# Kernel tuning notes

Measured on AMD Instinct MI355X. Metric: run time of the kernel, lower is better.

The kernel has to match this reference:

```python
import jax, jax.numpy as jnp
import numpy as np

B, N, C, H, W = 32, 32, 3, 32, 32
HID, OUT = 256, 128


def _conv(x, w, b):
    y = jax.lax.conv_general_dilated(
        x, w, window_strides=(1, 1), padding="SAME",
        dimension_numbers=("NCHW", "OIHW", "NCHW"))
    return y + b[None, :, None, None]


def _sage(h, lw, lb, rw):
    # PyG SAGEConv with mean aggregation on a fully-connected graph (no self-loops):
    # agg_i = (sum_j h_j - h_i) / (N-1); out = agg @ lw.T + lb + h @ rw.T
    n = h.shape[1]
    agg = (jnp.sum(h, axis=1, keepdims=True) - h) / (n - 1)
    return jnp.einsum('bnd,od->bno', agg, lw) + lb + jnp.einsum('bnd,od->bno', h, rw)


def setup_inputs() -> dict:
    key = jax.random.key(0)
    ks = jax.random.split(key, 16)
    def g(k, shape, scale):
        return jax.random.normal(k, shape, dtype=jnp.float32) * scale
    return {
        "x": jax.random.normal(ks[0], (B, N, C, H, W), dtype=jnp.float32),
        "mask": jnp.ones((B, N), dtype=jnp.float32),
        "conv1_w": g(ks[1], (64, C, 3, 3), 0.1),
        "conv1_b": jnp.zeros((64,), jnp.float32),
        "conv2_w": g(ks[2], (128, 64, 3, 3), 0.05),
        "conv2_b": jnp.zeros((128,), jnp.float32),
        "fc_w": g(ks[3], (HID, 128), 0.08),
        "fc_b": jnp.zeros((HID,), jnp.float32),
        "s1_lw": g(ks[4], (HID, HID), 0.06),
        "s1_lb": jnp.zeros((HID,), jnp.float32),
        "s1_rw": g(ks[5], (HID, HID), 0.06),
        "s2_lw": g(ks[6], (OUT, HID), 0.06),
        "s2_lb": jnp.zeros((OUT,), jnp.float32),
        "s2_rw": g(ks[7], (OUT, HID), 0.06),
    }


def reference(x, mask, conv1_w, conv1_b, conv2_w, conv2_b, fc_w, fc_b,
              s1_lw, s1_lb, s1_rw, s2_lw, s2_lb, s2_rw):
    b, n, c, h, w = x.shape
    z = x.reshape(b * n, c, h, w)
    z = jax.nn.relu(_conv(z, conv1_w, conv1_b))
    z = jax.nn.relu(_conv(z, conv2_w, conv2_b))
    z = jnp.mean(z, axis=(2, 3))                      # AdaptiveAvgPool2d((1,1)) + flatten
    z = z @ fc_w.T + fc_b                             # [B*N, HID]
    z = z.reshape(b, n, -1) * mask[:, :, None]
    z = jax.nn.relu(_sage(z, s1_lw, s1_lb, s1_rw))
    z = _sage(z, s2_lw, s2_lb, s2_rw)                 # [B, N, OUT]
    return z
```

## Files before the change

### kernel.cpp

```cpp
#include <hip/hip_runtime.h>
#include <hip/hip_bf16.h>


typedef __attribute__((ext_vector_type(8))) short bfrag;
typedef __attribute__((ext_vector_type(4))) float f32x4;
typedef __attribute__((ext_vector_type(16))) float f32x16;

static __device__ __forceinline__ unsigned short f2bf(float f) {
    union { float f; unsigned u; } v; v.f = f;
    unsigned r = v.u + 0x7fff + ((v.u >> 16) & 1);
    return (unsigned short)(r >> 16);
}

__global__ __launch_bounds__(256) void prep_kernel(
    const float* __restrict__ s1lw, const float* __restrict__ s1rw,
    const float* __restrict__ s2lw, const float* __restrict__ s2rw,
    const float* __restrict__ c2w, const float* __restrict__ c1w,
    const float* __restrict__ c1b, const float* __restrict__ fcw,
    float* __restrict__ l1T, float* __restrict__ w1pT,
    float* __restrict__ l2T, float* __restrict__ w2pT,
    float* __restrict__ fwT,
    short* __restrict__ w2c, short* __restrict__ w1b) {
    int i = blockIdx.x * 256 + threadIdx.x;
    const float inv31 = 1.f / 31.f;
    if (i < 65536) {
        int d = i >> 8, o = i & 255;
        float lw = s1lw[o * 256 + d];
        l1T[i]  = lw;
        w1pT[i] = s1rw[o * 256 + d] - lw * inv31;
    }
    if (i < 32768) {
        int d = i >> 7, o = i & 127;
        float lw = s2lw[o * 256 + d];
        l2T[i]  = lw;
        w2pT[i] = s2rw[o * 256 + d] - lw * inv31;
        int c = i >> 8, o2 = i & 255;
        fwT[i] = fcw[o2 * 128 + c];
    }
    if (i < 73728) {
        int tap = i >> 13, r = i & 8191;
        int ks = r >> 11, hi = (r >> 10) & 1, oc = (r >> 3) & 127, j = i & 7;
        int ic = ks * 16 + hi * 8 + j;
        w2c[i] = (short)f2bf(c2w[(oc * 64 + ic) * 9 + tap]);
    }
    if (i < 2048) {
        int oc = i >> 5, k = i & 31;
        float v = (k < 27) ? c1w[oc * 27 + k] : (k == 27 ? c1b[oc] : 0.f);
        w1b[i] = (short)f2bf(v);
    }
}

__global__ __launch_bounds__(256, 2) void fused_conv_kernel(
    const float* __restrict__ x, const short* __restrict__ w1b,
    const short* __restrict__ w2c, const float* __restrict__ b2,
    float* __restrict__ pooled4) {
    const int band = blockIdx.x, img = blockIdx.y;
    __shared__ short xt[3 * 12 * 34];
    __shared__ short c1t[10 * 34 * 72];
    __shared__ float wsum[4][128];
    const int t = threadIdx.x;
    const int w = t >> 6, lane = t & 63;
    const int ln15 = lane & 15, q8 = (lane >> 4) * 8;
    const int ln31 = lane & 31, hi = lane >> 5;

    const float* xi = x + img * 3072;
    for (int idx = t; idx < 1224; idx += 256) {
        int c = idx / 408, rem = idx % 408, r = rem / 34, col = rem % 34;
        int y = band * 8 - 2 + r, xx = col - 1;
        float v = 0.f;
        if ((unsigned)y < 32u && (unsigned)xx < 32u) v = xi[c * 1024 + y * 32 + xx];
        xt[idx] = (short)f2bf(v);
    }
    {
        f32x4 z = {0.f, 0.f, 0.f, 0.f};
        for (int i = t; i < 180; i += 256) {
            int r = i / 18, rem = i % 18, side = rem / 9, q = rem % 9;
            *(f32x4*)(c1t + (r * 34 + side * 33) * 72 + q * 8) = z;
        }
    }
    bfrag b1f[4];
#pragma unroll
    for (int ot = 0; ot < 4; ++ot)
        b1f[ot] = *(const bfrag*)(w1b + (ot * 16 + ln15) * 32 + q8);

    int xOff[8]; int kMask[8]; int kOvr[8];
#pragma unroll
    for (int j = 0; j < 8; ++j) {
        int k = q8 + j;
        int c = (k * 57) >> 9;
        int rem = k - 9 * c;
        int dy = (rem * 11) >> 5;
        int dx = rem - 3 * dy;
        int cc = c < 3 ? c : 2;
        xOff[j] = cc * 408 + dy * 34 + dx;
        kMask[j] = (c < 3) ? 0xFFFF : 0;
        kOvr[j]  = (c < 3) ? 0 : (k == 27 ? 0x3F80 : 0);
    }
    __syncthreads();

#pragma unroll 1
    for (int pt = 0; pt < 5; ++pt) {
        const int tile = w * 5 + pt;
        const int posA = tile * 16 + ln15;
        const int baseA = (posA >> 5) * 34 + (posA & 31);
        bfrag a1f;
#pragma unroll
        for (int j = 0; j < 8; ++j)
            a1f[j] = (short)((xt[xOff[j] + baseA] & kMask[j]) | kOvr[j]);
        f32x4 acc1[4];
#pragma unroll
        for (int ot = 0; ot < 4; ++ot) {
#pragma unroll
            for (int rg = 0; rg < 4; ++rg) acc1[ot][rg] = 0.f;
            acc1[ot] = __builtin_amdgcn_mfma_f32_16x16x32_bf16(
                a1f, b1f[ot], acc1[ot], 0, 0, 0);
        }
#pragma unroll
        for (int rg = 0; rg < 4; ++rg) {
            int pos = tile * 16 + (lane >> 4) * 4 + rg;
            int r = pos >> 5, xc = pos & 31;
            int y = band * 8 - 1 + r;
            bool valid = (unsigned)y < 32u;
#pragma unroll
            for (int ot = 0; ot < 4; ++ot) {
                float v = fmaxf(acc1[ot][rg], 0.f);
                c1t[(r * 34 + xc + 1) * 72 + ot * 16 + ln15] =
                    valid ? (short)f2bf(v) : (short)0;
            }
        }
    }
    __syncthreads();

    float b2v[4];
#pragma unroll
    for (int ot = 0; ot < 4; ++ot) b2v[ot] = b2[ot * 32 + ln31];

    f32x16 acc[2][4];
#pragma unroll
    for (int pt = 0; pt < 2; ++pt)
#pragma unroll
        for (int ot = 0; ot < 4; ++ot)
#pragma unroll
            for (int rg = 0; rg < 16; ++rg) acc[pt][ot][rg] = 0.f;

    const int aB0 = (w * 2 * 34 + ln31) * 72 + hi * 8;
    const int aB1 = aB0 + 34 * 72;
    const short* bPtr = w2c + hi * 1024 + ln31 * 8;

    bfrag aX[4], bX[8], aY[4], bY[8];
    auto loadS = [&](bfrag* af, bfrag* bf, int st) {
        const int tap = st >> 1, kh = st & 1;
        const int dy = (tap * 11) >> 5, dx = tap - 3 * dy;
        const int dOff = (dy * 34 + dx) * 72 + kh * 32;
        af[0] = *(const bfrag*)&c1t[aB0 + dOff];
        af[1] = *(const bfrag*)&c1t[aB0 + dOff + 16];
        af[2] = *(const bfrag*)&c1t[aB1 + dOff];
        af[3] = *(const bfrag*)&c1t[aB1 + dOff + 16];
        const short* p = bPtr + st * 4096;
#pragma unroll
        for (int kk = 0; kk < 2; ++kk)
#pragma unroll
            for (int ot = 0; ot < 4; ++ot)
                bf[kk * 4 + ot] = *(const bfrag*)(p + kk * 2048 + ot * 256);
    };
    auto computeS = [&](const bfrag* af, const bfrag* bf) {
#pragma unroll
        for (int kk = 0; kk < 2; ++kk)
#pragma unroll
            for (int pt = 0; pt < 2; ++pt)
#pragma unroll
                for (int ot = 0; ot < 4; ++ot)
                    acc[pt][ot] = __builtin_amdgcn_mfma_f32_32x32x16_bf16(
                        af[pt * 2 + kk], bf[kk * 4 + ot], acc[pt][ot], 0, 0, 0);
    };

    loadS(aX, bX, 0);
#pragma unroll 1
    for (int st = 0; st < 18; st += 2) {
        loadS(aY, bY, st + 1);
        computeS(aX, bX);
        if (st + 2 < 18) loadS(aX, bX, st + 2);
        computeS(aY, bY);
    }

#pragma unroll
    for (int ot = 0; ot < 4; ++ot) {
        float s = 0.f;
#pragma unroll
        for (int pt = 0; pt < 2; ++pt)
#pragma unroll
            for (int rg = 0; rg < 16; ++rg)
                s += fmaxf(acc[pt][ot][rg] + b2v[ot], 0.f);
        s += __shfl_xor(s, 32, 64);
        if (lane < 32) wsum[w][ot * 32 + ln31] = s;
    }
    __syncthreads();
    if (t < 128) {
        pooled4[((size_t)img * 4 + band) * 128 + t] =
            wsum[0][t] + wsum[1][t] + wsum[2][t] + wsum[3][t];
    }
}

__global__ __launch_bounds__(256) void fc_kernel(
    const float* __restrict__ pooled4, const float* __restrict__ fwT,
    const float* __restrict__ fb, const float* __restrict__ mask,
    float* __restrict__ z1) {
    const int img = blockIdx.x;
    __shared__ float m[128];
    const int t = threadIdx.x;
    if (t < 128) {
        const float* p = pooled4 + (size_t)img * 4 * 128 + t;
        m[t] = (p[0] + p[128] + p[256] + p[384]) * (1.f / 1024.f);
    }
    __syncthreads();
    float acc = fb[t];
#pragma unroll 4
    for (int c = 0; c < 128; ++c) acc = fmaf(m[c], fwT[c * 256 + t], acc);
    z1[img * 256 + t] = acc * mask[img];
}

__global__ __launch_bounds__(256) void sage1_kernel(
    const float* __restrict__ z1, const float* __restrict__ l1T,
    const float* __restrict__ lb, const float* __restrict__ w1pT,
    float* __restrict__ z2) {
    const int bb = blockIdx.x >> 3, chunk = blockIdx.x & 7;
    __shared__ float h[32 * 256];
    __shared__ float sl[256];
    const int t = threadIdx.x;
    const float* zb = z1 + bb * 8192;
    for (int idx = t; idx < 8192; idx += 256) h[idx] = zb[idx];
    __syncthreads();
    float s = 0.f;
#pragma unroll
    for (int n = 0; n < 32; ++n) s += h[n * 256 + t];
    sl[t] = s * (1.f / 31.f);
    __syncthreads();
    float c = lb[t];
#pragma unroll 4
    for (int d = 0; d < 256; ++d) c = fmaf(sl[d], l1T[d * 256 + t], c);
    float acc[4];
#pragma unroll
    for (int i = 0; i < 4; ++i) acc[i] = c;
    for (int d0 = 0; d0 < 256; d0 += 4) {
        float wv0 = w1pT[(d0 + 0) * 256 + t];
        float wv1 = w1pT[(d0 + 1) * 256 + t];
        float wv2 = w1pT[(d0 + 2) * 256 + t];
        float wv3 = w1pT[(d0 + 3) * 256 + t];
#pragma unroll
        for (int i = 0; i < 4; ++i) {
            f32x4 hv = *(const f32x4*)&h[(chunk * 4 + i) * 256 + d0];
            acc[i] = fmaf(hv[0], wv0, acc[i]);
            acc[i] = fmaf(hv[1], wv1, acc[i]);
            acc[i] = fmaf(hv[2], wv2, acc[i]);
            acc[i] = fmaf(hv[3], wv3, acc[i]);
        }
    }
    for (int i = 0; i < 4; ++i)
        z2[(bb * 32 + chunk * 4 + i) * 256 + t] = fmaxf(acc[i], 0.f);
}

__global__ __launch_bounds__(256) void sage2_kernel(
    const float* __restrict__ z2, const float* __restrict__ l2T,
    const float* __restrict__ lb, const float* __restrict__ w2pT,
    float* __restrict__ out) {
    const int bb = blockIdx.x >> 3, chunk = blockIdx.x & 7;
    __shared__ float h[32 * 256];
    __shared__ float sl[256];
    const int t = threadIdx.x;
    const float* zb = z2 + bb * 8192;
    for (int idx = t; idx < 8192; idx += 256) h[idx] = zb[idx];
    __syncthreads();
    float s = 0.f;
#pragma unroll
    for (int n = 0; n < 32; ++n) s += h[n * 256 + t];
    sl[t] = s * (1.f / 31.f);
    __syncthreads();
    const int o = t & 127, half = t >> 7;
    float c = lb[o];
#pragma unroll 4
    for (int d = 0; d < 256; ++d) c = fmaf(sl[d], l2T[d * 128 + o], c);
    float acc[2];
    acc[0] = c; acc[1] = c;
    const int n0 = chunk * 4 + half * 2;
    for (int d0 = 0; d0 < 256; d0 += 4) {
        float wv0 = w2pT[(d0 + 0) * 128 + o];
        float wv1 = w2pT[(d0 + 1) * 128 + o];
        float wv2 = w2pT[(d0 + 2) * 128 + o];
        float wv3 = w2pT[(d0 + 3) * 128 + o];
#pragma unroll
        for (int ii = 0; ii < 2; ++ii) {
            f32x4 hv = *(const f32x4*)&h[(n0 + ii) * 256 + d0];
            acc[ii] = fmaf(hv[0], wv0, acc[ii]);
            acc[ii] = fmaf(hv[1], wv1, acc[ii]);
            acc[ii] = fmaf(hv[2], wv2, acc[ii]);
            acc[ii] = fmaf(hv[3], wv3, acc[ii]);
        }
    }
    for (int ii = 0; ii < 2; ++ii)
        out[(size_t)(bb * 32 + n0 + ii) * 128 + o] = acc[ii];
}

extern "C" void kernel_launch(void* const* d_in, const int* in_sizes, int n_in,
                              void* d_out, int out_size, void* d_ws, size_t ws_size,
                              hipStream_t stream) {
    const float* x    = (const float*)d_in[0];
    const float* mask = (const float*)d_in[1];
    const float* c1w  = (const float*)d_in[2];
    const float* c1b  = (const float*)d_in[3];
    const float* c2w  = (const float*)d_in[4];
    const float* c2b  = (const float*)d_in[5];
    const float* fcw  = (const float*)d_in[6];
    const float* fcb  = (const float*)d_in[7];
    const float* s1lw = (const float*)d_in[8];
    const float* s1lb = (const float*)d_in[9];
    const float* s1rw = (const float*)d_in[10];
    const float* s2lw = (const float*)d_in[11];
    const float* s2lb = (const float*)d_in[12];
    const float* s2rw = (const float*)d_in[13];
    float* out = (float*)d_out;

    char* ws = (char*)d_ws;
    float* pooled4 = (float*)(ws);
    float* z1      = (float*)(ws + 2048u * 1024);
    float* z2      = (float*)(ws + 3072u * 1024);
    float* l1T     = (float*)(ws + 4096u * 1024);
    float* w1pT    = (float*)(ws + 4352u * 1024);
    float* l2T     = (float*)(ws + 4608u * 1024);
    float* w2pT    = (float*)(ws + 4736u * 1024);
    float* fwT     = (float*)(ws + 4864u * 1024);
    short* w2c     = (short*)(ws + 4992u * 1024);
    short* w1b     = (short*)(ws + 5136u * 1024);

    prep_kernel<<<dim3(288), 256, 0, stream>>>(s1lw, s1rw, s2lw, s2rw, c2w, c1w, c1b,
                                               fcw, l1T, w1pT, l2T, w2pT, fwT, w2c, w1b);
    fused_conv_kernel<<<dim3(4, 1024), 256, 0, stream>>>(x, w1b, w2c, c2b, pooled4);
    fc_kernel<<<dim3(1024), 256, 0, stream>>>(pooled4, fwT, fcb, mask, z1);
    sage1_kernel<<<dim3(256), 256, 0, stream>>>(z1, l1T, s1lb, w1pT, z2);
    sage2_kernel<<<dim3(256), 256, 0, stream>>>(z2, l2T, s2lb, w2pT, out);
}
```

Before: 288.3 us.

## Halve conv band height, accumulate pooled sums atomically, batch fc over images

```diff
diff --git a/kernel.cpp b/kernel.cpp
--- a/kernel.cpp
+++ b/kernel.cpp
@@ -20,7 +20,8 @@
     float* __restrict__ l1T, float* __restrict__ w1pT,
     float* __restrict__ l2T, float* __restrict__ w2pT,
     float* __restrict__ fwT,
-    short* __restrict__ w2c, short* __restrict__ w1b) {
+    short* __restrict__ w2c, short* __restrict__ w1b,
+    float* __restrict__ pooled) {
     int i = blockIdx.x * 256 + threadIdx.x;
     const float inv31 = 1.f / 31.f;
     if (i < 65536) {
@@ -28,6 +29,8 @@
         float lw = s1lw[o * 256 + d];
         l1T[i]  = lw;
         w1pT[i] = s1rw[o * 256 + d] - lw * inv31;
+        pooled[i] = 0.f;
+        pooled[i + 65536] = 0.f;
     }
     if (i < 32768) {
         int d = i >> 7, o = i & 127;
@@ -50,13 +53,13 @@
     }
 }
 
-__global__ __launch_bounds__(256, 2) void fused_conv_kernel(
+__global__ __launch_bounds__(256, 3) void fused_conv_kernel(
     const float* __restrict__ x, const short* __restrict__ w1b,
     const short* __restrict__ w2c, const float* __restrict__ b2,
-    float* __restrict__ pooled4) {
+    float* __restrict__ pooled) {
     const int band = blockIdx.x, img = blockIdx.y;
-    __shared__ short xt[3 * 12 * 34];
-    __shared__ short c1t[10 * 34 * 72];
+    __shared__ short xt[3 * 8 * 34];
+    __shared__ short c1t[6 * 34 * 72];
     __shared__ float wsum[4][128];
     const int t = threadIdx.x;
     const int w = t >> 6, lane = t & 63;
@@ -64,16 +67,16 @@
     const int ln31 = lane & 31, hi = lane >> 5;
 
     const float* xi = x + img * 3072;
-    for (int idx = t; idx < 1224; idx += 256) {
-        int c = idx / 408, rem = idx % 408, r = rem / 34, col = rem % 34;
-        int y = band * 8 - 2 + r, xx = col - 1;
+    for (int idx = t; idx < 816; idx += 256) {
+        int c = idx / 272, rem = idx % 272, r = rem / 34, col = rem % 34;
+        int y = band * 4 - 2 + r, xx = col - 1;
         float v = 0.f;
         if ((unsigned)y < 32u && (unsigned)xx < 32u) v = xi[c * 1024 + y * 32 + xx];
         xt[idx] = (short)f2bf(v);
     }
     {
         f32x4 z = {0.f, 0.f, 0.f, 0.f};
-        for (int i = t; i < 180; i += 256) {
+        for (int i = t; i < 108; i += 256) {
             int r = i / 18, rem = i % 18, side = rem / 9, q = rem % 9;
             *(f32x4*)(c1t + (r * 34 + side * 33) * 72 + q * 8) = z;
         }
@@ -92,15 +95,15 @@
         int dy = (rem * 11) >> 5;
         int dx = rem - 3 * dy;
         int cc = c < 3 ? c : 2;
-        xOff[j] = cc * 408 + dy * 34 + dx;
+        xOff[j] = cc * 272 + dy * 34 + dx;
         kMask[j] = (c < 3) ? 0xFFFF : 0;
         kOvr[j]  = (c < 3) ? 0 : (k == 27 ? 0x3F80 : 0);
     }
     __syncthreads();
 
 #pragma unroll 1
-    for (int pt = 0; pt < 5; ++pt) {
-        const int tile = w * 5 + pt;
+    for (int pt = 0; pt < 3; ++pt) {
+        const int tile = w * 3 + pt;
         const int posA = tile * 16 + ln15;
         const int baseA = (posA >> 5) * 34 + (posA & 31);
         bfrag a1f;
@@ -119,7 +122,7 @@
         for (int rg = 0; rg < 4; ++rg) {
             int pos = tile * 16 + (lane >> 4) * 4 + rg;
             int r = pos >> 5, xc = pos & 31;
-            int y = band * 8 - 1 + r;
+            int y = band * 4 - 1 + r;
             bool valid = (unsigned)y < 32u;
 #pragma unroll
             for (int ot = 0; ot < 4; ++ot) {
@@ -135,27 +138,17 @@
 #pragma unroll
     for (int ot = 0; ot < 4; ++ot) b2v[ot] = b2[ot * 32 + ln31];
 
-    f32x16 acc[2][4];
-#pragma unroll
-    for (int pt = 0; pt < 2; ++pt)
-#pragma unroll
-        for (int ot = 0; ot < 4; ++ot)
-#pragma unroll
-            for (int rg = 0; rg < 16; ++rg) acc[pt][ot][rg] = 0.f;
-
-    const int aB0 = (w * 2 * 34 + ln31) * 72 + hi * 8;
-    const int aB1 = aB0 + 34 * 72;
+    f32x16 acc[4];
+#pragma unroll
+    for (int ot = 0; ot < 4; ++ot)
+#pragma unroll
+        for (int rg = 0; rg < 16; ++rg) acc[ot][rg] = 0.f;
+
+    const int aB0 = (w * 34 + ln31) * 72 + hi * 8;
     const short* bPtr = w2c + hi * 1024 + ln31 * 8;
 
-    bfrag aX[4], bX[8], aY[4], bY[8];
-    auto loadS = [&](bfrag* af, bfrag* bf, int st) {
-        const int tap = st >> 1, kh = st & 1;
-        const int dy = (tap * 11) >> 5, dx = tap - 3 * dy;
-        const int dOff = (dy * 34 + dx) * 72 + kh * 32;
-        af[0] = *(const bfrag*)&c1t[aB0 + dOff];
-        af[1] = *(const bfrag*)&c1t[aB0 + dOff + 16];
-        af[2] = *(const bfrag*)&c1t[aB1 + dOff];
-        af[3] = *(const bfrag*)&c1t[aB1 + dOff + 16];
+    bfrag bX[8], bY[8];
+    auto loadB = [&](bfrag* bf, int st) {
         const short* p = bPtr + st * 4096;
 #pragma unroll
         for (int kk = 0; kk < 2; ++kk)
@@ -163,60 +156,73 @@
             for (int ot = 0; ot < 4; ++ot)
                 bf[kk * 4 + ot] = *(const bfrag*)(p + kk * 2048 + ot * 256);
     };
-    auto computeS = [&](const bfrag* af, const bfrag* bf) {
-#pragma unroll
-        for (int kk = 0; kk < 2; ++kk)
-#pragma unroll
-            for (int pt = 0; pt < 2; ++pt)
-#pragma unroll
-                for (int ot = 0; ot < 4; ++ot)
-                    acc[pt][ot] = __builtin_amdgcn_mfma_f32_32x32x16_bf16(
-                        af[pt * 2 + kk], bf[kk * 4 + ot], acc[pt][ot], 0, 0, 0);
+    auto computeS = [&](int st, const bfrag* bf) {
+        const int tap = st >> 1, kh = st & 1;
+        const int dy = (tap * 11) >> 5, dx = tap - 3 * dy;
+        const int a0 = aB0 + (dy * 34 + dx) * 72 + kh * 32;
+        bfrag af0 = *(const bfrag*)&c1t[a0];
+        bfrag af1 = *(const bfrag*)&c1t[a0 + 16];
+#pragma unroll
+        for (int ot = 0; ot < 4; ++ot)
+            acc[ot] = __builtin_amdgcn_mfma_f32_32x32x16_bf16(
+                af0, bf[ot], acc[ot], 0, 0, 0);
+#pragma unroll
+        for (int ot = 0; ot < 4; ++ot)
+            acc[ot] = __builtin_amdgcn_mfma_f32_32x32x16_bf16(
+                af1, bf[4 + ot], acc[ot], 0, 0, 0);
     };
 
-    loadS(aX, bX, 0);
+    loadB(bX, 0);
 #pragma unroll 1
     for (int st = 0; st < 18; st += 2) {
-        loadS(aY, bY, st + 1);
-        computeS(aX, bX);
-        if (st + 2 < 18) loadS(aX, bX, st + 2);
-        computeS(aY, bY);
+        loadB(bY, st + 1);
+        computeS(st, bX);
+        if (st + 2 < 18) loadB(bX, st + 2);
+        computeS(st + 1, bY);
     }
 
 #pragma unroll
     for (int ot = 0; ot < 4; ++ot) {
         float s = 0.f;
 #pragma unroll
-        for (int pt = 0; pt < 2; ++pt)
-#pragma unroll
-            for (int rg = 0; rg < 16; ++rg)
-                s += fmaxf(acc[pt][ot][rg] + b2v[ot], 0.f);
+        for (int rg = 0; rg < 16; ++rg)
+            s += fmaxf(acc[ot][rg] + b2v[ot], 0.f);
         s += __shfl_xor(s, 32, 64);
         if (lane < 32) wsum[w][ot * 32 + ln31] = s;
     }
     __syncthreads();
     if (t < 128) {
-        pooled4[((size_t)img * 4 + band) * 128 + t] =
-            wsum[0][t] + wsum[1][t] + wsum[2][t] + wsum[3][t];
+        atomicAdd(&pooled[(size_t)img * 128 + t],
+                  wsum[0][t] + wsum[1][t] + wsum[2][t] + wsum[3][t]);
     }
 }
 
 __global__ __launch_bounds__(256) void fc_kernel(
-    const float* __restrict__ pooled4, const float* __restrict__ fwT,
+    const float* __restrict__ pooled, const float* __restrict__ fwT,
     const float* __restrict__ fb, const float* __restrict__ mask,
     float* __restrict__ z1) {
-    const int img = blockIdx.x;
-    __shared__ float m[128];
+    const int g = blockIdx.x;
+    __shared__ float m[4][128];
     const int t = threadIdx.x;
     if (t < 128) {
-        const float* p = pooled4 + (size_t)img * 4 * 128 + t;
-        m[t] = (p[0] + p[128] + p[256] + p[384]) * (1.f / 1024.f);
-    }
-    __syncthreads();
-    float acc = fb[t];
+#pragma unroll
+        for (int i = 0; i < 4; ++i)
+            m[i][t] = pooled[(size_t)(g * 4 + i) * 128 + t] * (1.f / 1024.f);
+    }
+    __syncthreads();
+    float a0 = fb[t], a1 = a0, a2 = a0, a3 = a0;
 #pragma unroll 4
-    for (int c = 0; c < 128; ++c) acc = fmaf(m[c], fwT[c * 256 + t], acc);
-    z1[img * 256 + t] = acc * mask[img];
+    for (int c = 0; c < 128; ++c) {
+        float wv = fwT[c * 256 + t];
+        a0 = fmaf(m[0][c], wv, a0);
+        a1 = fmaf(m[1][c], wv, a1);
+        a2 = fmaf(m[2][c], wv, a2);
+        a3 = fmaf(m[3][c], wv, a3);
+    }
+    z1[(g * 4 + 0) * 256 + t] = a0 * mask[g * 4 + 0];
+    z1[(g * 4 + 1) * 256 + t] = a1 * mask[g * 4 + 1];
+    z1[(g * 4 + 2) * 256 + t] = a2 * mask[g * 4 + 2];
+    z1[(g * 4 + 3) * 256 + t] = a3 * mask[g * 4 + 3];
 }
 
 __global__ __launch_bounds__(256) void sage1_kernel(
@@ -320,7 +326,7 @@
     float* out = (float*)d_out;
 
     char* ws = (char*)d_ws;
-    float* pooled4 = (float*)(ws);
+    float* pooled  = (float*)(ws);
     float* z1      = (float*)(ws + 2048u * 1024);
     float* z2      = (float*)(ws + 3072u * 1024);
     float* l1T     = (float*)(ws + 4096u * 1024);
@@ -332,9 +338,10 @@
     short* w1b     = (short*)(ws + 5136u * 1024);
 
     prep_kernel<<<dim3(288), 256, 0, stream>>>(s1lw, s1rw, s2lw, s2rw, c2w, c1w, c1b,
-                                               fcw, l1T, w1pT, l2T, w2pT, fwT, w2c, w1b);
-    fused_conv_kernel<<<dim3(4, 1024), 256, 0, stream>>>(x, w1b, w2c, c2b, pooled4);
-    fc_kernel<<<dim3(1024), 256, 0, stream>>>(pooled4, fwT, fcb, mask, z1);
+                                               fcw, l1T, w1pT, l2T, w2pT, fwT, w2c, w1b,
+                                               pooled);
+    fused_conv_kernel<<<dim3(8, 1024), 256, 0, stream>>>(x, w1b, w2c, c2b, pooled);
+    fc_kernel<<<dim3(256), 256, 0, stream>>>(pooled, fwT, fcb, mask, z1);
     sage1_kernel<<<dim3(256), 256, 0, stream>>>(z1, l1T, s1lb, w1pT, z2);
     sage2_kernel<<<dim3(256), 256, 0, stream>>>(z2, l2T, s2lb, w2pT, out);
 }
```

New measurement: 313.1 us. +8.6%, slower.

## Stage conv2 weights through triple-buffered LDS and pack conv1 bf16 stores

Applied to the files above, without the earlier changes.

```diff
diff --git a/kernel.cpp b/kernel.cpp
--- a/kernel.cpp
+++ b/kernel.cpp
@@ -10,6 +10,18 @@
     union { float f; unsigned u; } v; v.f = f;
     unsigned r = v.u + 0x7fff + ((v.u >> 16) & 1);
     return (unsigned short)(r >> 16);
+}
+
+static __device__ __forceinline__ unsigned cvtpk(float lo, float hi) {
+    unsigned r;
+    asm("v_cvt_pk_bf16_f32 %0, %1, %2" : "=v"(r) : "v"(lo), "v"(hi));
+    return r;
+}
+
+static __device__ __forceinline__ void gl_lds16(const short* g, short* l) {
+    __builtin_amdgcn_global_load_lds(
+        (const __attribute__((address_space(1))) unsigned int*)g,
+        (__attribute__((address_space(3))) unsigned int*)l, 16, 0, 0);
 }
 
 __global__ __launch_bounds__(256) void prep_kernel(
@@ -57,6 +69,7 @@
     const int band = blockIdx.x, img = blockIdx.y;
     __shared__ short xt[3 * 12 * 34];
     __shared__ short c1t[10 * 34 * 72];
+    __shared__ short bufB[3][4096];
     __shared__ float wsum[4][128];
     const int t = threadIdx.x;
     const int w = t >> 6, lane = t & 63;
@@ -98,11 +111,20 @@
     }
     __syncthreads();
 
+    {
+        const short* src = w2c + t * 8;
+        short* dst = (short*)bufB + t * 8;
+        gl_lds16(src, dst);
+        gl_lds16(src + 2048, dst + 2048);
+        gl_lds16(src + 4096, dst + 4096);
+        gl_lds16(src + 6144, dst + 6144);
+    }
+
 #pragma unroll 1
     for (int pt = 0; pt < 5; ++pt) {
         const int tile = w * 5 + pt;
-        const int posA = tile * 16 + ln15;
-        const int baseA = (posA >> 5) * 34 + (posA & 31);
+        const int r = tile >> 1, xcb = (tile & 1) << 4;
+        const int baseA = r * 34 + xcb + ln15;
         bfrag a1f;
 #pragma unroll
         for (int j = 0; j < 8; ++j)
@@ -113,20 +135,19 @@
 #pragma unroll
             for (int rg = 0; rg < 4; ++rg) acc1[ot][rg] = 0.f;
             acc1[ot] = __builtin_amdgcn_mfma_f32_16x16x32_bf16(
-                a1f, b1f[ot], acc1[ot], 0, 0, 0);
-        }
-#pragma unroll
-        for (int rg = 0; rg < 4; ++rg) {
-            int pos = tile * 16 + (lane >> 4) * 4 + rg;
-            int r = pos >> 5, xc = pos & 31;
-            int y = band * 8 - 1 + r;
-            bool valid = (unsigned)y < 32u;
-#pragma unroll
-            for (int ot = 0; ot < 4; ++ot) {
-                float v = fmaxf(acc1[ot][rg], 0.f);
-                c1t[(r * 34 + xc + 1) * 72 + ot * 16 + ln15] =
-                    valid ? (short)f2bf(v) : (short)0;
+                b1f[ot], a1f, acc1[ot], 0, 0, 0);
+        }
+        const int y = band * 8 - 1 + r;
+        const bool valid = (unsigned)y < 32u;
+        const int waddr = (r * 34 + xcb + ln15 + 1) * 72 + (lane >> 4) * 4;
+#pragma unroll
+        for (int ot = 0; ot < 4; ++ot) {
+            uint2 pk = {0u, 0u};
+            if (valid) {
+                pk.x = cvtpk(fmaxf(acc1[ot][0], 0.f), fmaxf(acc1[ot][1], 0.f));
+                pk.y = cvtpk(fmaxf(acc1[ot][2], 0.f), fmaxf(acc1[ot][3], 0.f));
             }
+            *(uint2*)&c1t[waddr + ot * 16] = pk;
         }
     }
     __syncthreads();
@@ -145,42 +166,54 @@
 
     const int aB0 = (w * 2 * 34 + ln31) * 72 + hi * 8;
     const int aB1 = aB0 + 34 * 72;
-    const short* bPtr = w2c + hi * 1024 + ln31 * 8;
-
-    bfrag aX[4], bX[8], aY[4], bY[8];
-    auto loadS = [&](bfrag* af, bfrag* bf, int st) {
+    const int bOff = hi * 1024 + ln31 * 8;
+    const short* stSrc = w2c + t * 8;
+    short* stDst = (short*)bufB + t * 8;
+
+    int rb = 0;
+#pragma unroll 1
+    for (int st = 0; st < 18; ++st) {
+        if (st + 2 < 18) {
+            const int sb = (rb >= 1) ? rb - 1 : 2;
+            const short* src = stSrc + (st + 2) * 4096;
+            short* dst = stDst + sb * 4096;
+            gl_lds16(src, dst);
+            gl_lds16(src + 2048, dst + 2048);
+        }
         const int tap = st >> 1, kh = st & 1;
         const int dy = (tap * 11) >> 5, dx = tap - 3 * dy;
-        const int dOff = (dy * 34 + dx) * 72 + kh * 32;
-        af[0] = *(const bfrag*)&c1t[aB0 + dOff];
-        af[1] = *(const bfrag*)&c1t[aB0 + dOff + 16];
-        af[2] = *(const bfrag*)&c1t[aB1 + dOff];
-        af[3] = *(const bfrag*)&c1t[aB1 + dOff + 16];
-        const short* p = bPtr + st * 4096;
+        const int aOff = (dy * 34 + dx) * 72 + kh * 32;
+        const short* bc = (const short*)bufB + rb * 4096 + bOff;
+        bfrag af0 = *(const bfrag*)&c1t[aB0 + aOff];
+        bfrag af1 = *(const bfrag*)&c1t[aB0 + aOff + 16];
+        bfrag af2 = *(const bfrag*)&c1t[aB1 + aOff];
+        bfrag af3 = *(const bfrag*)&c1t[aB1 + aOff + 16];
+        bfrag bf[8];
 #pragma unroll
         for (int kk = 0; kk < 2; ++kk)
 #pragma unroll
             for (int ot = 0; ot < 4; ++ot)
-                bf[kk * 4 + ot] = *(const bfrag*)(p + kk * 2048 + ot * 256);
-    };
-    auto computeS = [&](const bfrag* af, const bfrag* bf) {
-#pragma unroll
-        for (int kk = 0; kk < 2; ++kk)
-#pragma unroll
-            for (int pt = 0; pt < 2; ++pt)
-#pragma unroll
-                for (int ot = 0; ot < 4; ++ot)
-                    acc[pt][ot] = __builtin_amdgcn_mfma_f32_32x32x16_bf16(
-                        af[pt * 2 + kk], bf[kk * 4 + ot], acc[pt][ot], 0, 0, 0);
-    };
-
-    loadS(aX, bX, 0);
-#pragma unroll 1
-    for (int st = 0; st < 18; st += 2) {
-        loadS(aY, bY, st + 1);
-        computeS(aX, bX);
-        if (st + 2 < 18) loadS(aX, bX, st + 2);
-        computeS(aY, bY);
+                bf[kk * 4 + ot] = *(const bfrag*)(bc + kk * 2048 + ot * 256);
+#pragma unroll
+        for (int ot = 0; ot < 4; ++ot)
+            acc[0][ot] = __builtin_amdgcn_mfma_f32_32x32x16_bf16(
+                af0, bf[ot], acc[0][ot], 0, 0, 0);
+#pragma unroll
+        for (int ot = 0; ot < 4; ++ot)
+            acc[0][ot] = __builtin_amdgcn_mfma_f32_32x32x16_bf16(
+                af1, bf[4 + ot], acc[0][ot], 0, 0, 0);
+#pragma unroll
+        for (int ot = 0; ot < 4; ++ot)
+            acc[1][ot] = __builtin_amdgcn_mfma_f32_32x32x16_bf16(
+                af2, bf[ot], acc[1][ot], 0, 0, 0);
+#pragma unroll
+        for (int ot = 0; ot < 4; ++ot)
+            acc[1][ot] = __builtin_amdgcn_mfma_f32_32x32x16_bf16(
+                af3, bf[4 + ot], acc[1][ot], 0, 0, 0);
+        if (st < 16) { asm volatile("s_waitcnt vmcnt(2)" ::: "memory"); }
+        else         { asm volatile("s_waitcnt vmcnt(0)" ::: "memory"); }
+        __builtin_amdgcn_s_barrier();
+        rb = (rb == 2) ? 0 : rb + 1;
     }
 
 #pragma unroll
```

Measured after the change: 284.9 us. No clear change (-1.2%).
